# Kernel optimization log

Hardware: AMD Instinct MI355X
Metric: run time of the kernel (lower is better)

The kernel has to match this reference:

```python
import jax, jax.numpy as jnp
import numpy as np

N = 50000
E = 800000
F_IN = 128
HID = 128
N_CLS = 32


def setup_inputs() -> dict:
    key = jax.random.key(0)
    ks = jax.random.split(key, 8)
    x = jax.random.normal(ks[0], (N, F_IN), dtype=jnp.float32)
    edge_index = jax.random.randint(ks[1], (2, E), 0, N, dtype=jnp.int32)
    batch = jnp.zeros((N,), dtype=jnp.int32)
    # GCNConv learned params (glorot-ish scale)
    W1 = jax.random.normal(ks[2], (F_IN, HID), dtype=jnp.float32) / np.sqrt(F_IN)
    b1 = jnp.zeros((HID,), dtype=jnp.float32)
    W2 = jax.random.normal(ks[3], (HID, HID), dtype=jnp.float32) / np.sqrt(HID)
    b2 = jnp.zeros((HID,), dtype=jnp.float32)
    W3 = jax.random.normal(ks[4], (HID, N_CLS), dtype=jnp.float32) / np.sqrt(HID)
    b3 = jnp.zeros((N_CLS,), dtype=jnp.float32)
    return {"x": x, "edge_index": edge_index, "batch": batch,
            "W1": W1, "b1": b1, "W2": W2, "b2": b2, "W3": W3, "b3": b3}


def _gcn_norm(edge_index, num_nodes):
    """Add self-loops and compute symmetric D^-1/2 (A+I) D^-1/2 edge weights."""
    loop = jnp.arange(num_nodes, dtype=edge_index.dtype)
    row = jnp.concatenate([edge_index[0], loop])  # source
    col = jnp.concatenate([edge_index[1], loop])  # destination
    ones = jnp.ones(row.shape[0], dtype=jnp.float32)
    deg = jax.ops.segment_sum(ones, col, num_segments=num_nodes)
    dinv = jnp.where(deg > 0, jax.lax.rsqrt(deg), 0.0)
    norm = dinv[row] * dinv[col]  # [E + N]
    return row, col, norm


def _gcn_conv(x, row, col, norm, W, b):
    h = x @ W                               # [N, out]
    msg = h[row] * norm[:, None]            # gather + scale, [E+N, out]
    out = jax.ops.segment_sum(msg, col, num_segments=x.shape[0])
    return out + b


def reference(x, edge_index, batch, W1, b1, W2, b2, W3, b3):
    # eval mode: dropout(p=0.2) is identity
    num_nodes = x.shape[0]
    row, col, norm = _gcn_norm(edge_index, num_nodes)
    h = jax.nn.relu(_gcn_conv(x, row, col, norm, W1, b1))
    h = jax.nn.relu(_gcn_conv(h, row, col, norm, W2, b2))
    out = _gcn_conv(h, row, col, norm, W3, b3)
    return out
```

## Files before the change

kernel.cpp:

```cpp
#include <hip/hip_runtime.h>
#include <math.h>


__global__ __launch_bounds__(256) void count_part_kernel(const int* __restrict__ col,
                                                         int* __restrict__ deg, int E, int n) {
    const int part = blockIdx.x & 7;
    const int nb = gridDim.x >> 3;
    const int chunk = blockIdx.x >> 3;
    const int lo = (int)(((long long)part * n) >> 3);
    const int hi = (int)(((long long)(part + 1) * n) >> 3);
    for (int e = chunk * 256 + threadIdx.x; e < E; e += nb * 256) {
        const int c = col[e];
        if (c >= lo && c < hi) atomicAdd(&deg[c], 1);
    }
}

__global__ __launch_bounds__(256) void scan1_kernel(const int* __restrict__ deg,
                                                    int* __restrict__ local,
                                                    int* __restrict__ blocksums, int n) {
    __shared__ int wsum[4];
    const int t = threadIdx.x;
    const int lane = t & 63;
    const int wv = t >> 6;
    const int base = blockIdx.x * 1024 + t * 4;
    int a0 = (base + 0 < n) ? deg[base + 0] : 0;
    int a1 = (base + 1 < n) ? deg[base + 1] : 0;
    int a2 = (base + 2 < n) ? deg[base + 2] : 0;
    int a3 = (base + 3 < n) ? deg[base + 3] : 0;
    const int tot = a0 + a1 + a2 + a3;
    int incl = tot;
#pragma unroll
    for (int off = 1; off < 64; off <<= 1) {
        int u = __shfl_up(incl, off);
        if (lane >= off) incl += u;
    }
    if (lane == 63) wsum[wv] = incl;
    __syncthreads();
    int woff = 0;
#pragma unroll
    for (int w = 0; w < 4; ++w) woff += (w < wv) ? wsum[w] : 0;
    const int excl = woff + incl - tot;
    if (base + 0 < n) local[base + 0] = excl;
    if (base + 1 < n) local[base + 1] = excl + a0;
    if (base + 2 < n) local[base + 2] = excl + a0 + a1;
    if (base + 3 < n) local[base + 3] = excl + a0 + a1 + a2;
    if (t == 255) blocksums[blockIdx.x] = woff + incl;
}

__global__ void scan2_kernel(const int* __restrict__ blocksums, int* __restrict__ blockoff,
                             int* __restrict__ rowptr, int nb, int n) {
    const int lane = threadIdx.x;
    int v = (lane < nb) ? blocksums[lane] : 0;
    int incl = v;
#pragma unroll
    for (int off = 1; off < 64; off <<= 1) {
        int u = __shfl_up(incl, off);
        if (lane >= off) incl += u;
    }
    if (lane < nb) blockoff[lane] = incl - v;
    if (lane == 63) rowptr[n] = incl;
}

__global__ void scan3_kernel(const int* __restrict__ local, const int* __restrict__ blockoff,
                             const int* __restrict__ deg, int* __restrict__ rowptr,
                             int* __restrict__ cursor, float* __restrict__ dinv, int n) {
    int i = blockIdx.x * blockDim.x + threadIdx.x;
    if (i < n) {
        const int v = local[i] + blockoff[i >> 10];
        rowptr[i] = v;
        cursor[i] = v;
        dinv[i] = rsqrtf((float)deg[i] + 1.0f);
    }
}

__global__ __launch_bounds__(256) void fill_part_kernel(const int* __restrict__ row,
                                                        const int* __restrict__ col,
                                                        int* __restrict__ cursor,
                                                        int* __restrict__ csr, int E, int n) {
    const int part = blockIdx.x & 7;
    const int nb = gridDim.x >> 3;
    const int chunk = blockIdx.x >> 3;
    const int lo = (int)(((long long)part * n) >> 3);
    const int hi = (int)(((long long)(part + 1) * n) >> 3);
    for (int e = chunk * 256 + threadIdx.x; e < E; e += nb * 256) {
        const int c = col[e];
        if (c >= lo && c < hi) {
            const int r = row[e];
            if ((unsigned)r < (unsigned)n) {
                const int pos = atomicAdd(&cursor[c], 1);
                csr[pos] = r;
            }
        }
    }
}

template <int OUT, int COLS>
__global__ __launch_bounds__(256) void gemm_kernel(const float* __restrict__ X,
                                                   const float* __restrict__ W,
                                                   const float* __restrict__ dinv,
                                                   float* __restrict__ out, int n) {
    constexpr int NSLAB = OUT / COLS;
    constexpr int CQ  = COLS / 4;
    constexpr int RG  = 256 / CQ;
    constexpr int R   = 4;
    constexpr int RPI = RG * R;
    __shared__ float Wl[128 * COLS];

    const int t = threadIdx.x;
    const int c0 = (int)(blockIdx.x % NSLAB) * COLS;
    const int rowblk = blockIdx.x / NSLAB;

    for (int i = t; i < 128 * CQ; i += 256) {
        const int k  = i / CQ;
        const int cc = i % CQ;
        ((float4*)Wl)[i] = *(const float4*)&W[(size_t)k * OUT + c0 + cc * 4];
    }
    __syncthreads();

    const int cq = t % CQ;
    const int rg = t / CQ;
    const float4* X4 = (const float4*)X;

    const int r0 = rowblk * RPI + rg * R;
    float4 acc[R];
#pragma unroll
    for (int r = 0; r < R; ++r) acc[r] = make_float4(0.f, 0.f, 0.f, 0.f);

    if (r0 + R <= n) {
#pragma unroll 4
        for (int k4 = 0; k4 < 32; ++k4) {
            const float* wp = &Wl[k4 * 4 * COLS + cq * 4];
            float4 w0 = *(const float4*)(wp);
            float4 w1 = *(const float4*)(wp + COLS);
            float4 w2 = *(const float4*)(wp + 2 * COLS);
            float4 w3 = *(const float4*)(wp + 3 * COLS);
#pragma unroll
            for (int r = 0; r < R; ++r) {
                float4 xv = X4[(size_t)(r0 + r) * 32 + k4];
                acc[r].x = fmaf(xv.x, w0.x, acc[r].x);
                acc[r].x = fmaf(xv.y, w1.x, acc[r].x);
                acc[r].x = fmaf(xv.z, w2.x, acc[r].x);
                acc[r].x = fmaf(xv.w, w3.x, acc[r].x);
                acc[r].y = fmaf(xv.x, w0.y, acc[r].y);
                acc[r].y = fmaf(xv.y, w1.y, acc[r].y);
                acc[r].y = fmaf(xv.z, w2.y, acc[r].y);
                acc[r].y = fmaf(xv.w, w3.y, acc[r].y);
                acc[r].z = fmaf(xv.x, w0.z, acc[r].z);
                acc[r].z = fmaf(xv.y, w1.z, acc[r].z);
                acc[r].z = fmaf(xv.z, w2.z, acc[r].z);
                acc[r].z = fmaf(xv.w, w3.z, acc[r].z);
                acc[r].w = fmaf(xv.x, w0.w, acc[r].w);
                acc[r].w = fmaf(xv.y, w1.w, acc[r].w);
                acc[r].w = fmaf(xv.z, w2.w, acc[r].w);
                acc[r].w = fmaf(xv.w, w3.w, acc[r].w);
            }
        }
#pragma unroll
        for (int r = 0; r < R; ++r) {
            const float s = dinv[r0 + r];
            acc[r].x *= s; acc[r].y *= s; acc[r].z *= s; acc[r].w *= s;
            *(float4*)&out[(size_t)(r0 + r) * OUT + c0 + cq * 4] = acc[r];
        }
    } else if (r0 < n) {
        for (int r = 0; r < R; ++r) {
            const int row = r0 + r;
            if (row >= n) break;
            float4 a = make_float4(0.f, 0.f, 0.f, 0.f);
            for (int k4 = 0; k4 < 32; ++k4) {
                float4 xv = X4[(size_t)row * 32 + k4];
                const float* wp = &Wl[k4 * 4 * COLS + cq * 4];
                float4 w0 = *(const float4*)(wp);
                float4 w1 = *(const float4*)(wp + COLS);
                float4 w2 = *(const float4*)(wp + 2 * COLS);
                float4 w3 = *(const float4*)(wp + 3 * COLS);
                a.x = fmaf(xv.x, w0.x, a.x); a.x = fmaf(xv.y, w1.x, a.x);
                a.x = fmaf(xv.z, w2.x, a.x); a.x = fmaf(xv.w, w3.x, a.x);
                a.y = fmaf(xv.x, w0.y, a.y); a.y = fmaf(xv.y, w1.y, a.y);
                a.y = fmaf(xv.z, w2.y, a.y); a.y = fmaf(xv.w, w3.y, a.y);
                a.z = fmaf(xv.x, w0.z, a.z); a.z = fmaf(xv.y, w1.z, a.z);
                a.z = fmaf(xv.z, w2.z, a.z); a.z = fmaf(xv.w, w3.z, a.z);
                a.w = fmaf(xv.x, w0.w, a.w); a.w = fmaf(xv.y, w1.w, a.w);
                a.w = fmaf(xv.z, w2.w, a.w); a.w = fmaf(xv.w, w3.w, a.w);
            }
            const float s = dinv[row];
            a.x *= s; a.y *= s; a.z *= s; a.w *= s;
            *(float4*)&out[(size_t)row * OUT + c0 + cq * 4] = a;
        }
    }
}

template <int F, bool RELU>
__global__ __launch_bounds__(256) void agg_kernel(const float* __restrict__ hs,
                                                  const int* __restrict__ rowptr,
                                                  const int* __restrict__ csr,
                                                  const float* __restrict__ dinv,
                                                  const float* __restrict__ bias,
                                                  float* __restrict__ out, int n) {
    constexpr int LPN = F / 4;
    constexpr int NPB = 256 / LPN;
    constexpr int F4  = F / 4;
    const int t = threadIdx.x;
    const int node = blockIdx.x * NPB + t / LPN;
    const int fo = t % LPN;
    if (node >= n) return;

    const float4* h4 = (const float4*)hs;
    float4 self = h4[(size_t)node * F4 + fo];
    float4 a[8];
#pragma unroll
    for (int j = 0; j < 8; ++j) a[j] = make_float4(0.f, 0.f, 0.f, 0.f);

    const int s = rowptr[node];
    const int e = rowptr[node + 1];
    for (int i = s; i < e; i += 8) {
        int   idx[8];
        float msk[8];
#pragma unroll
        for (int j = 0; j < 8; ++j) {
            const int k = i + j;
            const int kc = (k < e) ? k : (e - 1);
            idx[j] = csr[kc];
            msk[j] = (k < e) ? 1.f : 0.f;
        }
#pragma unroll
        for (int j = 0; j < 8; ++j) {
            float4 v = h4[(size_t)idx[j] * F4 + fo];
            a[j].x = fmaf(v.x, msk[j], a[j].x);
            a[j].y = fmaf(v.y, msk[j], a[j].y);
            a[j].z = fmaf(v.z, msk[j], a[j].z);
            a[j].w = fmaf(v.w, msk[j], a[j].w);
        }
    }
    float accx = self.x + ((a[0].x + a[1].x) + (a[2].x + a[3].x)) + ((a[4].x + a[5].x) + (a[6].x + a[7].x));
    float accy = self.y + ((a[0].y + a[1].y) + (a[2].y + a[3].y)) + ((a[4].y + a[5].y) + (a[6].y + a[7].y));
    float accz = self.z + ((a[0].z + a[1].z) + (a[2].z + a[3].z)) + ((a[4].z + a[5].z) + (a[6].z + a[7].z));
    float accw = self.w + ((a[0].w + a[1].w) + (a[2].w + a[3].w)) + ((a[4].w + a[5].w) + (a[6].w + a[7].w));
    const float dc = dinv[node];
    const float4 b = *(const float4*)&bias[fo * 4];
    float ox = fmaf(accx, dc, b.x);
    float oy = fmaf(accy, dc, b.y);
    float oz = fmaf(accz, dc, b.z);
    float ow = fmaf(accw, dc, b.w);
    if (RELU) {
        ox = fmaxf(ox, 0.f); oy = fmaxf(oy, 0.f);
        oz = fmaxf(oz, 0.f); ow = fmaxf(ow, 0.f);
    }
    float4 res = {ox, oy, oz, ow};
    *(float4*)&out[(size_t)node * F + fo * 4] = res;
}

extern "C" void kernel_launch(void* const* d_in, const int* in_sizes, int n_in,
                              void* d_out, int out_size, void* d_ws, size_t ws_size,
                              hipStream_t stream) {
    const float* x  = (const float*)d_in[0];
    const int*   ei = (const int*)d_in[1];
    const float* W1 = (const float*)d_in[3];
    const float* b1 = (const float*)d_in[4];
    const float* W2 = (const float*)d_in[5];
    const float* b2 = (const float*)d_in[6];
    const float* W3 = (const float*)d_in[7];
    const float* b3 = (const float*)d_in[8];
    float* out = (float*)d_out;

    const int N = in_sizes[0] / 128;
    const int E = in_sizes[1] / 2;
    const int* erow = ei;
    const int* ecol = ei + E;

    char* ws = (char*)d_ws;
    auto alloc = [&](size_t bytes) {
        char* p = ws;
        ws += (bytes + 255) & ~(size_t)255;
        return p;
    };
    int*   deg    = (int*)alloc((size_t)N * 4);
    int*   rowptr = (int*)alloc((size_t)(N + 1) * 4);
    int*   cursor = (int*)alloc((size_t)N * 4);
    int*   csr    = (int*)alloc((size_t)E * 4);
    float* dinv   = (float*)alloc((size_t)N * 4);
    float* buf1   = (float*)alloc((size_t)N * 128 * 4);
    float* buf2   = (float*)alloc((size_t)N * 128 * 4);

    int* local = (int*)buf1;
    int* bsums = local + N;
    int* boffs = bsums + 64;

    const int nb = (N + 1023) / 1024;

    hipMemsetAsync(deg, 0, (size_t)N * 4, stream);
    count_part_kernel<<<8 * 128, 256, 0, stream>>>(ecol, deg, E, N);
    scan1_kernel<<<nb, 256, 0, stream>>>(deg, local, bsums, N);
    scan2_kernel<<<1, 64, 0, stream>>>(bsums, boffs, rowptr, nb, N);
    scan3_kernel<<<(N + 255) / 256, 256, 0, stream>>>(local, boffs, deg, rowptr, cursor, dinv, N);
    fill_part_kernel<<<8 * 128, 256, 0, stream>>>(erow, ecol, cursor, csr, E, N);

    const int g128 = ((N + 63) / 64) * 2;
    const int g32  = (N + 127) / 128;

    gemm_kernel<128, 64><<<g128, 256, 0, stream>>>(x, W1, dinv, buf1, N);
    agg_kernel<128, true><<<(N + 7) / 8, 256, 0, stream>>>(buf1, rowptr, csr, dinv, b1, buf2, N);

    gemm_kernel<128, 64><<<g128, 256, 0, stream>>>(buf2, W2, dinv, buf1, N);
    agg_kernel<128, true><<<(N + 7) / 8, 256, 0, stream>>>(buf1, rowptr, csr, dinv, b2, buf2, N);

    gemm_kernel<32, 32><<<g32, 256, 0, stream>>>(buf2, W3, dinv, buf1, N);
    agg_kernel<32, false><<<(N + 31) / 32, 256, 0, stream>>>(buf1, rowptr, csr, dinv, b3, out, N);
}
```

Measured before the change: 316.9 us.

## Store hidden features in 16-column chunk-major layout for chunked aggregation

The 128-wide GEMMs now write their output in a column-chunk-major layout: 8 chunks of 16 floats, each chunk contiguous across all nodes. A new aggregation kernel gives each block one chunk and 64 nodes, so the gathered rows for that chunk sit in a working set of about 3.2 MB instead of the full 25.6 MB feature matrix. The aim is better L2 reuse on the random neighbor gathers. In exchange, each gather is only 64 bytes per neighbor, there are 8x more blocks each re-reading rowptr and csr, and neighbors are unrolled 8-wide with masked padding work.

After: 287.3 us. 9.3% less time.

```diff
diff --git a/kernel.cpp b/kernel.cpp
--- a/kernel.cpp
+++ b/kernel.cpp
@@ -94,7 +94,7 @@
     }
 }
 
-template <int OUT, int COLS>
+template <int OUT, int COLS, bool CM>
 __global__ __launch_bounds__(256) void gemm_kernel(const float* __restrict__ X,
                                                    const float* __restrict__ W,
                                                    const float* __restrict__ dinv,
@@ -120,6 +120,8 @@
     const int cq = t % CQ;
     const int rg = t / CQ;
     const float4* X4 = (const float4*)X;
+    const int gcol = c0 + cq * 4;
+    const size_t cm_base = (size_t)(gcol >> 4) * n * 16 + (gcol & 15);
 
     const int r0 = rowblk * RPI + rg * R;
     float4 acc[R];
@@ -159,7 +161,9 @@
         for (int r = 0; r < R; ++r) {
             const float s = dinv[r0 + r];
             acc[r].x *= s; acc[r].y *= s; acc[r].z *= s; acc[r].w *= s;
-            *(float4*)&out[(size_t)(r0 + r) * OUT + c0 + cq * 4] = acc[r];
+            float* dst = CM ? &out[cm_base + (size_t)(r0 + r) * 16]
+                            : &out[(size_t)(r0 + r) * OUT + gcol];
+            *(float4*)dst = acc[r];
         }
     } else if (r0 < n) {
         for (int r = 0; r < R; ++r) {
@@ -184,9 +188,71 @@
             }
             const float s = dinv[row];
             a.x *= s; a.y *= s; a.z *= s; a.w *= s;
-            *(float4*)&out[(size_t)row * OUT + c0 + cq * 4] = a;
-        }
-    }
+            float* dst = CM ? &out[cm_base + (size_t)row * 16]
+                            : &out[(size_t)row * OUT + gcol];
+            *(float4*)dst = a;
+        }
+    }
+}
+
+template <bool RELU>
+__global__ __launch_bounds__(256) void agg_chunk_kernel(const float* __restrict__ hc,
+                                                        const int* __restrict__ rowptr,
+                                                        const int* __restrict__ csr,
+                                                        const float* __restrict__ dinv,
+                                                        const float* __restrict__ bias,
+                                                        float* __restrict__ out, int n) {
+    const int t = threadIdx.x;
+    const int cc = blockIdx.x & 7;
+    const int g  = blockIdx.x >> 3;
+    const int node = g * 64 + (t >> 2);
+    const int fo = t & 3;
+    if (node >= n) return;
+
+    const float4* h4 = (const float4*)(hc + (size_t)cc * n * 16);
+    float4 self = h4[(size_t)node * 4 + fo];
+    float4 a[8];
+#pragma unroll
+    for (int j = 0; j < 8; ++j) a[j] = make_float4(0.f, 0.f, 0.f, 0.f);
+
+    const int s = rowptr[node];
+    const int e = rowptr[node + 1];
+    for (int i = s; i < e; i += 8) {
+        int   idx[8];
+        float msk[8];
+#pragma unroll
+        for (int j = 0; j < 8; ++j) {
+            const int k = i + j;
+            const int kc = (k < e) ? k : (e - 1);
+            idx[j] = csr[kc];
+            msk[j] = (k < e) ? 1.f : 0.f;
+        }
+#pragma unroll
+        for (int j = 0; j < 8; ++j) {
+            float4 v = h4[(size_t)idx[j] * 4 + fo];
+            a[j].x = fmaf(v.x, msk[j], a[j].x);
+            a[j].y = fmaf(v.y, msk[j], a[j].y);
+            a[j].z = fmaf(v.z, msk[j], a[j].z);
+            a[j].w = fmaf(v.w, msk[j], a[j].w);
+        }
+    }
+    float accx = self.x + ((a[0].x + a[1].x) + (a[2].x + a[3].x)) + ((a[4].x + a[5].x) + (a[6].x + a[7].x));
+    float accy = self.y + ((a[0].y + a[1].y) + (a[2].y + a[3].y)) + ((a[4].y + a[5].y) + (a[6].y + a[7].y));
+    float accz = self.z + ((a[0].z + a[1].z) + (a[2].z + a[3].z)) + ((a[4].z + a[5].z) + (a[6].z + a[7].z));
+    float accw = self.w + ((a[0].w + a[1].w) + (a[2].w + a[3].w)) + ((a[4].w + a[5].w) + (a[6].w + a[7].w));
+    const float dc = dinv[node];
+    const int f = cc * 16 + fo * 4;
+    const float4 b = *(const float4*)&bias[f];
+    float ox = fmaf(accx, dc, b.x);
+    float oy = fmaf(accy, dc, b.y);
+    float oz = fmaf(accz, dc, b.z);
+    float ow = fmaf(accw, dc, b.w);
+    if (RELU) {
+        ox = fmaxf(ox, 0.f); oy = fmaxf(oy, 0.f);
+        oz = fmaxf(oz, 0.f); ow = fmaxf(ow, 0.f);
+    }
+    float4 res = {ox, oy, oz, ow};
+    *(float4*)&out[(size_t)node * 128 + f] = res;
 }
 
 template <int F, bool RELU>
@@ -296,13 +362,14 @@
 
     const int g128 = ((N + 63) / 64) * 2;
     const int g32  = (N + 127) / 128;
-
-    gemm_kernel<128, 64><<<g128, 256, 0, stream>>>(x, W1, dinv, buf1, N);
-    agg_kernel<128, true><<<(N + 7) / 8, 256, 0, stream>>>(buf1, rowptr, csr, dinv, b1, buf2, N);
-
-    gemm_kernel<128, 64><<<g128, 256, 0, stream>>>(buf2, W2, dinv, buf1, N);
-    agg_kernel<128, true><<<(N + 7) / 8, 256, 0, stream>>>(buf1, rowptr, csr, dinv, b2, buf2, N);
-
-    gemm_kernel<32, 32><<<g32, 256, 0, stream>>>(buf2, W3, dinv, buf1, N);
+    const int gagg = ((N + 63) / 64) * 8;
+
+    gemm_kernel<128, 64, true><<<g128, 256, 0, stream>>>(x, W1, dinv, buf1, N);
+    agg_chunk_kernel<true><<<gagg, 256, 0, stream>>>(buf1, rowptr, csr, dinv, b1, buf2, N);
+
+    gemm_kernel<128, 64, true><<<g128, 256, 0, stream>>>(buf2, W2, dinv, buf1, N);
+    agg_chunk_kernel<true><<<gagg, 256, 0, stream>>>(buf1, rowptr, csr, dinv, b2, buf2, N);
+
+    gemm_kernel<32, 32, false><<<g32, 256, 0, stream>>>(buf2, W3, dinv, buf1, N);
     agg_kernel<32, false><<<(N + 31) / 32, 256, 0, stream>>>(buf1, rowptr, csr, dinv, b3, out, N);
 }
```

## Store GEMM output in 16-column chunk-major layout for cache-local aggregation

Applied to the files above, without the earlier changes.

The GEMM now writes its output in a column-chunked layout: contiguous slabs of 16 features per node, with each slab holding all nodes. The aggregation kernel is rewritten so that consecutive blocks handle different feature chunks of the same node group. Each chunk's gather working set (N×64 bytes) is then far smaller than the full row-major feature matrix, which should improve L2 hit rates for the random neighbour gathers. In exchange, every edge's CSR index is reloaded once per chunk, and each gather only fetches 64-byte segments.

Result: faster. 288.8 us (median of 3 runs) (-8.9%).

```diff
diff --git a/kernel.cpp b/kernel.cpp
--- a/kernel.cpp
+++ b/kernel.cpp
@@ -94,7 +94,7 @@
     }
 }
 
-template <int OUT, int COLS>
+template <int OUT, int COLS, bool CM>
 __global__ __launch_bounds__(256) void gemm_kernel(const float* __restrict__ X,
                                                    const float* __restrict__ W,
                                                    const float* __restrict__ dinv,
@@ -120,6 +120,8 @@
     const int cq = t % CQ;
     const int rg = t / CQ;
     const float4* X4 = (const float4*)X;
+    const int gcol = c0 + cq * 4;
+    const size_t cm_base = (size_t)(gcol >> 4) * n * 16 + (gcol & 15);
 
     const int r0 = rowblk * RPI + rg * R;
     float4 acc[R];
@@ -159,7 +161,9 @@
         for (int r = 0; r < R; ++r) {
             const float s = dinv[r0 + r];
             acc[r].x *= s; acc[r].y *= s; acc[r].z *= s; acc[r].w *= s;
-            *(float4*)&out[(size_t)(r0 + r) * OUT + c0 + cq * 4] = acc[r];
+            float* dst = CM ? &out[cm_base + (size_t)(r0 + r) * 16]
+                            : &out[(size_t)(r0 + r) * OUT + gcol];
+            *(float4*)dst = acc[r];
         }
     } else if (r0 < n) {
         for (int r = 0; r < R; ++r) {
@@ -184,28 +188,33 @@
             }
             const float s = dinv[row];
             a.x *= s; a.y *= s; a.z *= s; a.w *= s;
-            *(float4*)&out[(size_t)row * OUT + c0 + cq * 4] = a;
-        }
-    }
-}
-
-template <int F, bool RELU>
-__global__ __launch_bounds__(256) void agg_kernel(const float* __restrict__ hs,
-                                                  const int* __restrict__ rowptr,
-                                                  const int* __restrict__ csr,
-                                                  const float* __restrict__ dinv,
-                                                  const float* __restrict__ bias,
-                                                  float* __restrict__ out, int n) {
-    constexpr int LPN = F / 4;
-    constexpr int NPB = 256 / LPN;
-    constexpr int F4  = F / 4;
+            float* dst = CM ? &out[cm_base + (size_t)row * 16]
+                            : &out[(size_t)row * OUT + gcol];
+            *(float4*)dst = a;
+        }
+    }
+}
+
+template <int NC, bool RELU>
+__global__ __launch_bounds__(256) void agg_chunk_kernel(const float* __restrict__ hc,
+                                                        const int* __restrict__ rowptr,
+                                                        const int* __restrict__ csr,
+                                                        const float* __restrict__ dinv,
+                                                        const float* __restrict__ bias,
+                                                        float* __restrict__ out, int n) {
+    constexpr int F = NC * 16;
+    constexpr int NSPLIT = 8 / NC;
     const int t = threadIdx.x;
-    const int node = blockIdx.x * NPB + t / LPN;
-    const int fo = t % LPN;
+    const int slot = blockIdx.x & 7;
+    const int cc = slot % NC;
+    const int split = slot / NC;
+    const int g = (blockIdx.x >> 3) * NSPLIT + split;
+    const int node = g * 64 + (t >> 2);
+    const int fo = t & 3;
     if (node >= n) return;
 
-    const float4* h4 = (const float4*)hs;
-    float4 self = h4[(size_t)node * F4 + fo];
+    const float4* h4 = (const float4*)(hc + (size_t)cc * n * 16);
+    float4 self = h4[(size_t)node * 4 + fo];
     float4 a[8];
 #pragma unroll
     for (int j = 0; j < 8; ++j) a[j] = make_float4(0.f, 0.f, 0.f, 0.f);
@@ -224,7 +233,7 @@
         }
 #pragma unroll
         for (int j = 0; j < 8; ++j) {
-            float4 v = h4[(size_t)idx[j] * F4 + fo];
+            float4 v = h4[(size_t)idx[j] * 4 + fo];
             a[j].x = fmaf(v.x, msk[j], a[j].x);
             a[j].y = fmaf(v.y, msk[j], a[j].y);
             a[j].z = fmaf(v.z, msk[j], a[j].z);
@@ -236,7 +245,8 @@
     float accz = self.z + ((a[0].z + a[1].z) + (a[2].z + a[3].z)) + ((a[4].z + a[5].z) + (a[6].z + a[7].z));
     float accw = self.w + ((a[0].w + a[1].w) + (a[2].w + a[3].w)) + ((a[4].w + a[5].w) + (a[6].w + a[7].w));
     const float dc = dinv[node];
-    const float4 b = *(const float4*)&bias[fo * 4];
+    const int f = cc * 16 + fo * 4;
+    const float4 b = *(const float4*)&bias[f];
     float ox = fmaf(accx, dc, b.x);
     float oy = fmaf(accy, dc, b.y);
     float oz = fmaf(accz, dc, b.z);
@@ -246,7 +256,7 @@
         oz = fmaxf(oz, 0.f); ow = fmaxf(ow, 0.f);
     }
     float4 res = {ox, oy, oz, ow};
-    *(float4*)&out[(size_t)node * F + fo * 4] = res;
+    *(float4*)&out[(size_t)node * F + f] = res;
 }
 
 extern "C" void kernel_launch(void* const* d_in, const int* in_sizes, int n_in,
@@ -294,15 +304,18 @@
     scan3_kernel<<<(N + 255) / 256, 256, 0, stream>>>(local, boffs, deg, rowptr, cursor, dinv, N);
     fill_part_kernel<<<8 * 128, 256, 0, stream>>>(erow, ecol, cursor, csr, E, N);
 
+    const int ngroups = (N + 63) / 64;
     const int g128 = ((N + 63) / 64) * 2;
     const int g32  = (N + 127) / 128;
-
-    gemm_kernel<128, 64><<<g128, 256, 0, stream>>>(x, W1, dinv, buf1, N);
-    agg_kernel<128, true><<<(N + 7) / 8, 256, 0, stream>>>(buf1, rowptr, csr, dinv, b1, buf2, N);
-
-    gemm_kernel<128, 64><<<g128, 256, 0, stream>>>(buf2, W2, dinv, buf1, N);
-    agg_kernel<128, true><<<(N + 7) / 8, 256, 0, stream>>>(buf1, rowptr, csr, dinv, b2, buf2, N);
-
-    gemm_kernel<32, 32><<<g32, 256, 0, stream>>>(buf2, W3, dinv, buf1, N);
-    agg_kernel<32, false><<<(N + 31) / 32, 256, 0, stream>>>(buf1, rowptr, csr, dinv, b3, out, N);
-}
+    const int gagg8 = ngroups * 8;
+    const int gagg2 = ((ngroups + 3) / 4) * 8;
+
+    gemm_kernel<128, 64, true><<<g128, 256, 0, stream>>>(x, W1, dinv, buf1, N);
+    agg_chunk_kernel<8, true><<<gagg8, 256, 0, stream>>>(buf1, rowptr, csr, dinv, b1, buf2, N);
+
+    gemm_kernel<128, 64, true><<<g128, 256, 0, stream>>>(buf2, W2, dinv, buf1, N);
+    agg_chunk_kernel<8, true><<<gagg8, 256, 0, stream>>>(buf1, rowptr, csr, dinv, b2, buf2, N);
+
+    gemm_kernel<32, 32, true><<<g32, 256, 0, stream>>>(buf2, W3, dinv, buf1, N);
+    agg_chunk_kernel<2, false><<<gagg2, 256, 0, stream>>>(buf1, rowptr, csr, dinv, b3, out, N);
+}
```
